# Optimization experiments

Hardware: AMD Instinct MI355X
Metric: run time of the kernel (lower is better)

The kernel has to match this reference:

```python
import jax, jax.numpy as jnp
import numpy as np

N = 10000      # atoms
F = 32         # nr_atom_basis
H = 7          # nr_heads
C = F * H      # nr_coefficients = 224
E = 200000     # edges
NRBF = 50
CUTOFF = 5.0
EPS = 1e-8


def _seg_sum(x, idx, n):
    return jax.ops.segment_sum(x, idx, num_segments=n)


def _seg_mean(x, idx, n):
    # torch scatter_reduce 'mean' with include_self=False: sum/count, 0 for empty segments
    s = _seg_sum(x, idx, n)
    cnt = _seg_sum(jnp.ones((x.shape[0],), x.dtype), idx, n)
    cnt = jnp.maximum(cnt, 1.0).reshape((n,) + (1,) * (x.ndim - 1))
    return s / cnt


def _scatter_softmax(w, idx, n):
    m = jax.ops.segment_max(w, idx, num_segments=n)
    m = jnp.where(jnp.isfinite(m), m, 0.0)  # guard empty segments
    e = jnp.exp(w - m[idx])
    s = _seg_sum(e, idx, n)
    return e / s[idx]


def setup_inputs():
    key = jax.random.key(0)
    ks = jax.random.split(key, 16)
    def w(k, shape, scale=0.1):
        return jax.random.normal(k, shape, jnp.float32) * scale
    return {
        "h": w(ks[0], (N, F), 1.0),
        "x": w(ks[1], (N, 3), 1.0),
        "v": w(ks[2], (N, 3), 0.1),
        "pairlist": jax.random.randint(ks[3], (2, E), 0, N),
        "w_in": w(ks[4], (2 * F, NRBF)), "b_in": jnp.zeros((NRBF,), jnp.float32),
        "w_e1": w(ks[5], (2 * F + NRBF + 1, F)), "b_e1": jnp.zeros((F,), jnp.float32),
        "w_e2": w(ks[6], (F, F)), "b_e2": jnp.zeros((F,), jnp.float32),
        "w_att": w(ks[7], (F, H)), "b_att": jnp.zeros((H,), jnp.float32),
        "w_n1": w(ks[8], (F + C + F, F)), "b_n1": jnp.zeros((F,), jnp.float32),
        "w_n2": w(ks[9], (F, F)), "b_n2": jnp.zeros((F,), jnp.float32),
        "w_pn1": w(ks[10], (C, F)), "b_pn1": jnp.zeros((F,), jnp.float32),
        "w_pn2": w(ks[11], (F, F)), "b_pn2": jnp.zeros((F,), jnp.float32),
        "w_v1": w(ks[12], (F, F)), "b_v1": jnp.zeros((F,), jnp.float32),
        "w_v2": w(ks[13], (F, 1)),
        "w_xmix": w(ks[14], (C, C)),
        "w_vmix": w(ks[15], (C, 1)),
    }


def reference(h, x, v, pairlist, w_in, b_in, w_e1, b_e1, w_e2, b_e2,
              w_att, b_att, w_n1, b_n1, w_n2, b_n2, w_pn1, b_pn1,
              w_pn2, b_pn2, w_v1, b_v1, w_v2, w_xmix, w_vmix):
    act = jax.nn.silu
    idx_i, idx_j = pairlist[0], pairlist[1]
    n = h.shape[0]

    r_ij = x[idx_j] - x[idx_i]                      # [E,3]
    d_ij = jnp.linalg.norm(r_ij, axis=-1)           # [E]
    dir_ij = r_ij / (d_ij[:, None] + EPS)           # [E,3]

    # edge model: continuous-filter conv with concatenation
    h_cat = jnp.concatenate([h[idx_i], h[idx_j]], axis=-1)           # [E,2F]
    centers = jnp.linspace(0.0, CUTOFF, NRBF)
    width = centers[1] - centers[0]
    rbf = jnp.exp(-0.5 * ((d_ij[:, None] - centers) / width) ** 2)   # [E,NRBF]
    filt = rbf * (h_cat @ w_in + b_in)                               # [E,NRBF]
    edge_in = jnp.concatenate([h_cat, filt, d_ij[:, None]], axis=-1)
    h_ij_edge = act(edge_in @ w_e1 + b_e1) @ w_e2 + b_e2             # [E,F]

    # semantic attention (scatter softmax over edges grouped by idx_i)
    att_w = jax.nn.celu(h_ij_edge @ w_att + b_att, alpha=2.0)        # [E,H]
    cut = 0.5 * (jnp.cos(jnp.pi * d_ij / CUTOFF) + 1.0) * (d_ij < CUTOFF)
    att = _scatter_softmax(att_w * cut[:, None], idx_i, n)           # [E,H]
    # einsum('pf,ph->pfh').reshape -> f-major, h-minor
    h_ij_sem = (h_ij_edge[:, :, None] * att[:, None, :]).reshape(-1, C)  # [E,C]
    h_i_sem = _seg_sum(h_ij_sem, idx_i, n)                           # [N,C]

    # equivariant combinations + spatial attention
    comb = jnp.tanh(h_ij_sem @ w_xmix)[:, :, None] * dir_ij[:, None, :]  # [E,C,3]
    comb_mean = _seg_mean(comb, idx_i, n)                            # [N,C,3]
    cnsq = jnp.sum(comb_mean ** 2, axis=-1)                          # [N,C]
    h_i_spatial = act(act(cnsq @ w_pn1 + b_pn1) @ w_pn2 + b_pn2)     # [N,F]

    # node update
    node_in = jnp.concatenate([h, h_i_sem, h_i_spatial], axis=-1)
    h_upd = h + act(act(node_in @ w_n1 + b_n1) @ w_n2 + b_n2)        # [N,F]

    # velocity update
    v_ij = jnp.einsum('ecx,c->ex', comb, w_vmix[:, 0])               # [E,3]
    dv = _seg_mean(v_ij, idx_i, n)                                   # [N,3]
    gate = 2.0 * jax.nn.sigmoid(act(h @ w_v1 + b_v1) @ w_v2)         # [N,1]
    v_upd = gate * v + dv
    x_upd = x + v_upd
    return h_upd, x_upd, v_upd
```

## Files before the change

kernel.cpp:

```cpp
#include <hip/hip_runtime.h>
#include <math.h>

typedef unsigned short u16;
typedef __attribute__((ext_vector_type(8))) short bf16x8;
typedef __attribute__((ext_vector_type(4))) float f32x4;

constexpr int kF    = 32;
constexpr int kH    = 7;
constexpr int kC    = 224;
constexpr int kRBF  = 50;
constexpr int kM    = 128;
constexpr int kStr  = 232;
constexpr int kEM   = 128;
constexpr int kAStr = 136;
constexpr int kBStr = 40;
constexpr float kCut = 5.0f;
constexpr float kEps = 1e-8f;

__device__ __forceinline__ float silu_f(float a) { return a / (1.f + __expf(-a)); }
__device__ __forceinline__ float tanh_f(float x) {
    x = fminf(fmaxf(x, -15.f), 15.f);
    float e = __expf(2.f * x);
    return (e - 1.f) / (e + 1.f);
}
__device__ __forceinline__ float bf2f(u16 u) {
    union { unsigned int i; float f; } v; v.i = ((unsigned int)u) << 16; return v.f;
}
__device__ __forceinline__ u16 f2bf(float f) {
    union { float f; unsigned int i; } v; v.f = f;
    unsigned int x = v.i;
    unsigned int round = ((x >> 16) & 1u) + 0x7fffu;
    return (u16)((x + round) >> 16);
}
__device__ __forceinline__ unsigned pk2(float a, float b) {
    return (unsigned)f2bf(a) | ((unsigned)f2bf(b) << 16);
}

__global__ __launch_bounds__(256) void init_kernel(
    const float* __restrict__ wx, const float* __restrict__ w_in,
    const float* __restrict__ w_e1, const float* __restrict__ w_e2,
    const float* __restrict__ w_att, const float* __restrict__ b_e2,
    const float* __restrict__ b_att,
    u16* __restrict__ wxT, u16* __restrict__ W1T, u16* __restrict__ W2T,
    u16* __restrict__ W3T, u16* __restrict__ W24T, float* __restrict__ b24,
    int* __restrict__ counts, int* __restrict__ cursor, int N_)
{
    int idx = blockIdx.x * 256 + threadIdx.x;
    if (idx < kC * kC) {
        int c = idx / kC, k = idx - c * kC;
        wxT[idx] = f2bf(wx[k * kC + c]);
    }
    if (idx < N_) { counts[idx] = 0; cursor[idx] = 0; }

    if (blockIdx.x == 0) {
        int t = threadIdx.x;
        for (int i = t; i < 64 * 64; i += 256) {
            int n = i >> 6, k = i & 63;
            W1T[i] = f2bf((n < kRBF) ? w_in[k * kRBF + n] : 0.f);
        }
        for (int i = t; i < 32 * 128; i += 256) {
            int n = i >> 7, k = i & 127;
            W2T[i] = f2bf((k < 115) ? w_e1[k * kF + n] : 0.f);
        }
        for (int i = t; i < 32 * 32; i += 256) {
            int n = i >> 5, k = i & 31;
            W3T[i] = f2bf(w_e2[k * kF + n]);
        }
        for (int i = t; i < 16 * 32; i += 256) {
            int n = i >> 5, k = i & 31;
            float a = 0.f;
            if (n < kH) for (int o = 0; o < kF; o++) a += w_e2[k * kF + o] * w_att[o * kH + n];
            W24T[i] = f2bf(a);
        }
        if (t < kH) {
            float a = b_att[t];
            for (int o = 0; o < kF; o++) a += b_e2[o] * w_att[o * kH + t];
            b24[t] = a;
        }
    }
}

__global__ __launch_bounds__(256) void edge_kernel(
    const float* __restrict__ h, const float* __restrict__ x,
    const int* __restrict__ pl, int E_,
    const float* __restrict__ b_in, const float* __restrict__ b_e1,
    const float* __restrict__ b_e2,
    const u16* __restrict__ W1T, const u16* __restrict__ W2T,
    const u16* __restrict__ W3T, const u16* __restrict__ W24T,
    const float* __restrict__ b24,
    float* __restrict__ he_g, float* __restrict__ logit_g,
    float* __restrict__ dir_g, int* __restrict__ counts)
{
    __shared__ __align__(16) u16 s_A[kEM][kAStr];
    __shared__ __align__(16) u16 s_t1[kEM][kBStr];
    __shared__ float s_d[kEM];

    int t = threadIdx.x;
    int T0 = blockIdx.x * kEM;
    int w = t >> 6, lane = t & 63, quad = lane >> 4, l15 = lane & 15;

    {
        int e = t >> 1, half = t & 1;
        int ge = T0 + e;
        bool val = ge < E_;
        int i = 0, j = 0;
        if (val) { i = pl[ge]; j = pl[E_ + ge]; }
        const float4* pi = (const float4*)(h + (size_t)i * kF) + half * 4;
        const float4* pj = (const float4*)(h + (size_t)j * kF) + half * 4;
#pragma unroll
        for (int q = 0; q < 4; q++) {
            float4 a = val ? pi[q] : make_float4(0.f, 0.f, 0.f, 0.f);
            float4 b = val ? pj[q] : make_float4(0.f, 0.f, 0.f, 0.f);
            unsigned* di = (unsigned*)&s_A[e][half * 16 + 4 * q];
            di[0] = pk2(a.x, a.y); di[1] = pk2(a.z, a.w);
            unsigned* dj = (unsigned*)&s_A[e][kF + half * 16 + 4 * q];
            dj[0] = pk2(b.x, b.y); dj[1] = pk2(b.z, b.w);
        }
        if (half == 0) {
            float d = 0.f;
            if (val) {
                float r0 = x[j * 3 + 0] - x[i * 3 + 0];
                float r1 = x[j * 3 + 1] - x[i * 3 + 1];
                float r2 = x[j * 3 + 2] - x[i * 3 + 2];
                d = sqrtf(r0 * r0 + r1 * r1 + r2 * r2);
                float inv = 1.0f / (d + kEps);
                dir_g[(size_t)ge * 3 + 0] = r0 * inv;
                dir_g[(size_t)ge * 3 + 1] = r1 * inv;
                dir_g[(size_t)ge * 3 + 2] = r2 * inv;
                atomicAdd(&counts[i], 1);
            }
            s_d[e] = d;
            s_A[e][114] = f2bf(d);
            s_A[e][115] = 0;
            unsigned* z = (unsigned*)&s_A[e][116];
#pragma unroll
            for (int q = 0; q < 6; q++) z[q] = 0u;
        }
    }
    __syncthreads();

    const float invw = 49.0f / kCut;

    {
        bf16x8 a1[2][2];
#pragma unroll
        for (int rt = 0; rt < 2; rt++)
#pragma unroll
            for (int kt = 0; kt < 2; kt++)
                a1[rt][kt] = *(const bf16x8*)&s_A[32 * w + 16 * rt + l15][kt * 32 + quad * 8];
#pragma unroll
        for (int ct = 0; ct < 4; ct++) {
            int c = ct * 16 + l15;
            bf16x8 b0 = *(const bf16x8*)(W1T + (size_t)c * 64 + quad * 8);
            bf16x8 b1 = *(const bf16x8*)(W1T + (size_t)c * 64 + 32 + quad * 8);
            float bin = (c < kRBF) ? b_in[c] : 0.f;
#pragma unroll
            for (int rt = 0; rt < 2; rt++) {
                f32x4 acc = {0.f, 0.f, 0.f, 0.f};
                acc = __builtin_amdgcn_mfma_f32_16x16x32_bf16(a1[rt][0], b0, acc, 0, 0, 0);
                acc = __builtin_amdgcn_mfma_f32_16x16x32_bf16(a1[rt][1], b1, acc, 0, 0, 0);
                if (c < kRBF) {
#pragma unroll
                    for (int r = 0; r < 4; r++) {
                        int row = 32 * w + 16 * rt + quad * 4 + r;
                        float arg = s_d[row] * invw - (float)c;
                        float filt = __expf(-0.5f * arg * arg) * (acc[r] + bin);
                        s_A[row][64 + c] = f2bf(filt);
                    }
                }
            }
        }
    }

    {
        bf16x8 a2[2][4];
#pragma unroll
        for (int rt = 0; rt < 2; rt++)
#pragma unroll
            for (int kt = 0; kt < 4; kt++)
                a2[rt][kt] = *(const bf16x8*)&s_A[32 * w + 16 * rt + l15][kt * 32 + quad * 8];
#pragma unroll
        for (int ct = 0; ct < 2; ct++) {
            int c = ct * 16 + l15;
            bf16x8 bb[4];
#pragma unroll
            for (int kt = 0; kt < 4; kt++)
                bb[kt] = *(const bf16x8*)(W2T + (size_t)c * 128 + kt * 32 + quad * 8);
            float be = b_e1[c];
#pragma unroll
            for (int rt = 0; rt < 2; rt++) {
                f32x4 acc = {0.f, 0.f, 0.f, 0.f};
#pragma unroll
                for (int kt = 0; kt < 4; kt++)
                    acc = __builtin_amdgcn_mfma_f32_16x16x32_bf16(a2[rt][kt], bb[kt], acc, 0, 0, 0);
#pragma unroll
                for (int r = 0; r < 4; r++) {
                    int row = 32 * w + 16 * rt + quad * 4 + r;
                    s_t1[row][c] = f2bf(silu_f(acc[r] + be));
                }
            }
        }
    }

    {
        bf16x8 a3[2];
#pragma unroll
        for (int rt = 0; rt < 2; rt++)
            a3[rt] = *(const bf16x8*)&s_t1[32 * w + 16 * rt + l15][quad * 8];

#pragma unroll
        for (int ct = 0; ct < 2; ct++) {
            int c = ct * 16 + l15;
            bf16x8 b3 = *(const bf16x8*)(W3T + (size_t)c * 32 + quad * 8);
            float be = b_e2[c];
#pragma unroll
            for (int rt = 0; rt < 2; rt++) {
                f32x4 acc = {0.f, 0.f, 0.f, 0.f};
                acc = __builtin_amdgcn_mfma_f32_16x16x32_bf16(a3[rt], b3, acc, 0, 0, 0);
#pragma unroll
                for (int r = 0; r < 4; r++) {
                    int row = 32 * w + 16 * rt + quad * 4 + r;
                    int ge = T0 + row;
                    if (ge < E_) he_g[(size_t)ge * kF + c] = acc[r] + be;
                }
            }
        }
        {
            bf16x8 b4 = *(const bf16x8*)(W24T + (size_t)l15 * 32 + quad * 8);
            float bb = (l15 < kH) ? b24[l15] : 0.f;
#pragma unroll
            for (int rt = 0; rt < 2; rt++) {
                f32x4 acc = {0.f, 0.f, 0.f, 0.f};
                acc = __builtin_amdgcn_mfma_f32_16x16x32_bf16(a3[rt], b4, acc, 0, 0, 0);
                if (l15 < kH) {
#pragma unroll
                    for (int r = 0; r < 4; r++) {
                        int row = 32 * w + 16 * rt + quad * 4 + r;
                        int ge = T0 + row;
                        if (ge < E_) {
                            float a = acc[r] + bb;
                            a = (a >= 0.f) ? a : 2.f * (__expf(0.5f * a) - 1.f);
                            float dd = s_d[row];
                            float cut = (dd < kCut)
                                ? 0.5f * (__cosf(0.62831853071795864f * dd) + 1.f) : 0.f;
                            logit_g[(size_t)ge * kH + l15] = a * cut;
                        }
                    }
                }
            }
        }
    }
}

__global__ __launch_bounds__(1024) void scan_kernel(
    const int* __restrict__ counts, int* __restrict__ offsets, int n)
{
    __shared__ int buf[1024];
    int t = threadIdx.x;
    int chunk = (n + 1023) >> 10;
    int lo = t * chunk;
    int s = 0;
    for (int i = 0; i < chunk; i++) {
        int g = lo + i;
        if (g < n) s += counts[g];
    }
    buf[t] = s;
    __syncthreads();
    for (int off = 1; off < 1024; off <<= 1) {
        int v = (t >= off) ? buf[t - off] : 0;
        __syncthreads();
        buf[t] += v;
        __syncthreads();
    }
    int run = buf[t] - s;
    for (int i = 0; i < chunk; i++) {
        int g = lo + i;
        if (g < n) { offsets[g] = run; run += counts[g]; }
    }
    if (t == 1023) offsets[n] = buf[1023];
}

__global__ __launch_bounds__(256) void scatter_kernel(
    const int* __restrict__ pl, const int* __restrict__ offsets,
    int* __restrict__ cursor, int* __restrict__ sorted, int E_)
{
    int e = blockIdx.x * 256 + threadIdx.x;
    if (e < E_) {
        int i = pl[e];
        int p = atomicAdd(&cursor[i], 1);
        sorted[offsets[i] + p] = e;
    }
}

__global__ __launch_bounds__(256) void stats_kernel(
    const float* __restrict__ logit_g, const int* __restrict__ offsets,
    const int* __restrict__ sorted,
    float* __restrict__ m_g, float* __restrict__ invs_g, int N_)
{
    int wave = threadIdx.x >> 6;
    int lane = threadIdx.x & 63;
    int node = blockIdx.x * 4 + wave;
    if (node >= N_) return;
    int base = offsets[node];
    int deg  = offsets[node + 1] - base;

    float m[kH], ss[kH];
#pragma unroll
    for (int hh = 0; hh < kH; hh++) { m[hh] = -1e30f; ss[hh] = 0.f; }
    for (int e = lane; e < deg; e += 64) {
        int ed = sorted[base + e];
        const float* lp = logit_g + (size_t)ed * kH;
#pragma unroll
        for (int hh = 0; hh < kH; hh++) {
            float vv = lp[hh];
            if (vv > m[hh]) { ss[hh] *= __expf(m[hh] - vv); m[hh] = vv; }
            ss[hh] += __expf(vv - m[hh]);
        }
    }
#pragma unroll
    for (int hh = 0; hh < kH; hh++) {
        float mm = m[hh], s2 = ss[hh];
#pragma unroll
        for (int off = 32; off >= 1; off >>= 1) {
            float mo = __shfl_xor(mm, off);
            float so = __shfl_xor(s2, off);
            float mn = fmaxf(mm, mo);
            s2 = s2 * __expf(mm - mn) + so * __expf(mo - mn);
            mm = mn;
        }
        if (lane == 0) {
            m_g[(size_t)node * kH + hh] = mm;
            invs_g[(size_t)node * kH + hh] = (s2 > 0.f) ? 1.f / s2 : 0.f;
        }
    }
}

__global__ __launch_bounds__(256) void xmix_kernel(
    const float* __restrict__ he_g, const float* __restrict__ logit_g,
    const float* __restrict__ dir_g,
    const int* __restrict__ pl, const int* __restrict__ sorted,
    const float* __restrict__ m_g, const float* __restrict__ invs_g,
    const u16* __restrict__ wxT, int E_,
    float* __restrict__ nodeacc, float* __restrict__ bpart, int* __restrict__ bid)
{
    __shared__ __align__(16) u16 s_buf[kM][kStr];
    __shared__ float s_att[kM][kH];
    __shared__ __align__(16) float s_dir4[kM][4];
    __shared__ int   s_ed[kM];
    __shared__ int   s_node[kM];
    __shared__ int   s_prev, s_next;

    int t = threadIdx.x;
    int T0 = blockIdx.x * kM;
    int cp = min(kM, E_ - T0);

    if (t < kM) {
        int gi = T0 + t;
        int ed = (gi < E_) ? sorted[gi] : -1;
        s_ed[t] = ed;
        s_node[t] = (ed >= 0) ? pl[ed] : -1;
    }
    if (t == 0) {
        s_prev = (T0 > 0) ? pl[sorted[T0 - 1]] : -2;
        s_next = (T0 + cp < E_) ? pl[sorted[T0 + cp]] : -2;
    }
    __syncthreads();

    int w    = t >> 6;
    int lane = t & 63;
    int quad = lane >> 4;
    int l15  = lane & 15;

    int ws = 32 * w;
    int we = min(ws + 32, cp);
    bool winvalid = (ws < cp);
    bool contL = false, contR = false;
    if (winvalid) {
        int nfirst = s_node[ws], nlast = s_node[we - 1];
        contL = (w == 0) ? (s_prev == nfirst) : (s_node[ws - 1] == nfirst);
        contR = (we == cp) ? (s_next == nlast) : (s_node[we] == nlast);
    }
    if (lane == 0) {
        int b0 = -1, b1 = -1;
        if (winvalid) {
            int nfirst = s_node[ws], nlast = s_node[we - 1];
            b0 = contL ? nfirst : -1;
            if (contR && !(nfirst == nlast && contL)) b1 = nlast;
        }
        bid[8 * blockIdx.x + 2 * w + 0] = b0;
        bid[8 * blockIdx.x + 2 * w + 1] = b1;
    }
    bool active_w = winvalid && (lane < 56);
    int c0 = 4 * lane;

    for (int idx = t; idx < kM * kH; idx += 256) {
        int e = idx / kH, hh = idx - e * kH;
        int ed = s_ed[e];
        float a = 0.f;
        if (ed >= 0) {
            int nd = s_node[e];
            a = __expf(logit_g[(size_t)ed * kH + hh] - m_g[(size_t)nd * kH + hh])
                * invs_g[(size_t)nd * kH + hh];
        }
        s_att[e][hh] = a;
    }
    for (int idx = t; idx < cp * 3; idx += 256) {
        int e = idx / 3, xx = idx - e * 3;
        s_dir4[e][xx] = dir_g[(size_t)s_ed[e] * 3 + xx];
    }
    __syncthreads();

#pragma unroll
    for (int p = 0; p < kM * kF / 256; p++) {
        int idx = t + 256 * p;
        int e = idx >> 5, f = idx & 31;
        int ed = s_ed[e];
        float hv = (ed >= 0) ? he_g[(size_t)ed * kF + f] : 0.f;
        u16 sw[7];
#pragma unroll
        for (int hh = 0; hh < kH; hh++) sw[hh] = f2bf(hv * s_att[e][hh]);
        u16* dst = &s_buf[e][f * 7];
        if ((f & 1) == 0) {
            *(unsigned int*)(dst)     = (unsigned int)sw[0] | ((unsigned int)sw[1] << 16);
            *(unsigned int*)(dst + 2) = (unsigned int)sw[2] | ((unsigned int)sw[3] << 16);
            *(unsigned int*)(dst + 4) = (unsigned int)sw[4] | ((unsigned int)sw[5] << 16);
            dst[6] = sw[6];
        } else {
            dst[0] = sw[0];
            *(unsigned int*)(dst + 1) = (unsigned int)sw[1] | ((unsigned int)sw[2] << 16);
            *(unsigned int*)(dst + 3) = (unsigned int)sw[3] | ((unsigned int)sw[4] << 16);
            *(unsigned int*)(dst + 5) = (unsigned int)sw[5] | ((unsigned int)sw[6] << 16);
        }
    }
    __syncthreads();

    if (active_w) {
        float hs0 = 0.f, hs1 = 0.f, hs2 = 0.f, hs3 = 0.f;
        int rs = ws;
        for (int e = ws; e < we; e++) {
            if (s_node[e] != s_node[rs]) {
                bool comp = (rs > ws) || !contL;
                float4 vv = make_float4(hs0, hs1, hs2, hs3);
                if (comp) *(float4*)&nodeacc[(size_t)s_node[rs] * 896 + 672 + c0] = vv;
                else *(float4*)&bpart[(size_t)(8 * blockIdx.x + 2 * w) * 896 + 672 + c0] = vv;
                hs0 = hs1 = hs2 = hs3 = 0.f; rs = e;
            }
            uint2 pv = *(const uint2*)&s_buf[e][c0];
            hs0 += bf2f((u16)pv.x); hs1 += bf2f((u16)(pv.x >> 16));
            hs2 += bf2f((u16)pv.y); hs3 += bf2f((u16)(pv.y >> 16));
        }
        bool t0 = (rs == ws);
        bool comp = ((!t0) || !contL) && !contR;
        float4 vv = make_float4(hs0, hs1, hs2, hs3);
        if (comp) *(float4*)&nodeacc[(size_t)s_node[rs] * 896 + 672 + c0] = vv;
        else {
            int slot = (t0 && contL) ? 0 : 1;
            *(float4*)&bpart[(size_t)(8 * blockIdx.x + 2 * w + slot) * 896 + 672 + c0] = vv;
        }
    }

    bf16x8 afr[2][7];
#pragma unroll
    for (int rt = 0; rt < 2; rt++)
#pragma unroll
        for (int kt = 0; kt < 7; kt++)
            afr[rt][kt] = *(const bf16x8*)&s_buf[32 * w + 16 * rt + l15][kt * 32 + quad * 8];

    bf16x8 bA[7], bB[7];
    {
        const u16* bp = wxT + (size_t)l15 * kC + quad * 8;
#pragma unroll
        for (int kt = 0; kt < 7; kt++) bA[kt] = *(const bf16x8*)(bp + kt * 32);
    }
    __syncthreads();

    for (int ct = 0; ct < 14; ct++) {
        bf16x8* cur = (ct & 1) ? bB : bA;
        bf16x8* nxt = (ct & 1) ? bA : bB;
        if (ct < 13) {
            const u16* bp = wxT + (size_t)((ct + 1) * 16 + l15) * kC + quad * 8;
#pragma unroll
            for (int kt = 0; kt < 7; kt++) nxt[kt] = *(const bf16x8*)(bp + kt * 32);
        }
        f32x4 acc0 = {0.f, 0.f, 0.f, 0.f};
        f32x4 acc1 = {0.f, 0.f, 0.f, 0.f};
#pragma unroll
        for (int kt = 0; kt < 7; kt++) {
            acc0 = __builtin_amdgcn_mfma_f32_16x16x32_bf16(afr[0][kt], cur[kt], acc0, 0, 0, 0);
            acc1 = __builtin_amdgcn_mfma_f32_16x16x32_bf16(afr[1][kt], cur[kt], acc1, 0, 0, 0);
        }
        int colg = ct * 16 + l15;
#pragma unroll
        for (int s = 0; s < 2; s++) {
            f32x4 ac = s ? acc1 : acc0;
            int rbase = 32 * w + 16 * s + quad * 4;
#pragma unroll
            for (int r = 0; r < 4; r++)
                s_buf[rbase + r][colg] = f2bf(tanh_f(ac[r]));
        }
    }
    __syncthreads();

    if (active_w) {
        float a0[4] = {0.f, 0.f, 0.f, 0.f};
        float a1[4] = {0.f, 0.f, 0.f, 0.f};
        float a2[4] = {0.f, 0.f, 0.f, 0.f};
        int rs = ws;
        for (int e = ws; e < we; e++) {
            if (s_node[e] != s_node[rs]) {
                bool comp = (rs > ws) || !contL;
                float* p = comp ? (nodeacc + (size_t)s_node[rs] * 896)
                                : (bpart + (size_t)(8 * blockIdx.x + 2 * w) * 896);
                *(float4*)&p[c0]       = make_float4(a0[0], a0[1], a0[2], a0[3]);
                *(float4*)&p[224 + c0] = make_float4(a1[0], a1[1], a1[2], a1[3]);
                *(float4*)&p[448 + c0] = make_float4(a2[0], a2[1], a2[2], a2[3]);
#pragma unroll
                for (int q = 0; q < 4; q++) { a0[q] = 0.f; a1[q] = 0.f; a2[q] = 0.f; }
                rs = e;
            }
            float4 dd = *(const float4*)&s_dir4[e][0];
            uint2 pv = *(const uint2*)&s_buf[e][c0];
            float Tv[4];
            Tv[0] = bf2f((u16)pv.x); Tv[1] = bf2f((u16)(pv.x >> 16));
            Tv[2] = bf2f((u16)pv.y); Tv[3] = bf2f((u16)(pv.y >> 16));
#pragma unroll
            for (int q = 0; q < 4; q++) {
                a0[q] += Tv[q] * dd.x;
                a1[q] += Tv[q] * dd.y;
                a2[q] += Tv[q] * dd.z;
            }
        }
        bool t0 = (rs == ws);
        bool comp = ((!t0) || !contL) && !contR;
        float* p;
        if (comp) p = nodeacc + (size_t)s_node[rs] * 896;
        else {
            int slot = (t0 && contL) ? 0 : 1;
            p = bpart + (size_t)(8 * blockIdx.x + 2 * w + slot) * 896;
        }
        *(float4*)&p[c0]       = make_float4(a0[0], a0[1], a0[2], a0[3]);
        *(float4*)&p[224 + c0] = make_float4(a1[0], a1[1], a1[2], a1[3]);
        *(float4*)&p[448 + c0] = make_float4(a2[0], a2[1], a2[2], a2[3]);
    }
}

__global__ __launch_bounds__(256) void node_kernel(
    const float* __restrict__ h, const float* __restrict__ x, const float* __restrict__ v,
    const float* __restrict__ nodeacc, const float* __restrict__ bpart,
    const int* __restrict__ bid, const int* __restrict__ offs,
    const float* __restrict__ w_n1, const float* __restrict__ b_n1,
    const float* __restrict__ w_n2, const float* __restrict__ b_n2,
    const float* __restrict__ w_pn1, const float* __restrict__ b_pn1,
    const float* __restrict__ w_pn2, const float* __restrict__ b_pn2,
    const float* __restrict__ w_v1, const float* __restrict__ b_v1,
    const float* __restrict__ w_v2, const float* __restrict__ w_vmix,
    float* __restrict__ out_h, float* __restrict__ out_x, float* __restrict__ out_v,
    int N_)
{
    __shared__ float s_cm[4][3][kC];
    __shared__ float s_cnsq[4][kC];
    __shared__ float s_ni[4][288];
    __shared__ float s_part[8][4][kF];
    __shared__ float s_hn[4][kF], s_sp1[4][kF], s_spat[4][kF], s_n1v[4][kF], s_g1[4][kF];
    __shared__ float s_pdv[4][3][8];
    __shared__ float s_gate[4], s_dv[4][3];

    int t = threadIdx.x;
    int n0 = blockIdx.x * 4;

    if (t < kC) {
        for (int nd = 0; nd < 4; nd++) {
            int node = n0 + nd;
            if (node >= N_) break;
            int base = offs[node], end = offs[node + 1];
            int deg = end - base;
            float a0 = 0.f, a1 = 0.f, a2 = 0.f, hh = 0.f;
            if (deg > 0) {
                int wlo = base >> 5, whi = (end - 1) >> 5;
                if (wlo == whi) {
                    const float* p = nodeacc + (size_t)node * 896;
                    a0 = p[t]; a1 = p[224 + t]; a2 = p[448 + t]; hh = p[672 + t];
                } else {
                    for (int W = wlo; W <= whi; W++) {
#pragma unroll
                        for (int s = 0; s < 2; s++) {
                            if (bid[2 * W + s] == node) {
                                const float* p = bpart + (size_t)(2 * W + s) * 896;
                                a0 += p[t]; a1 += p[224 + t]; a2 += p[448 + t]; hh += p[672 + t];
                            }
                        }
                    }
                }
            }
            float invc = 1.f / fmaxf((float)deg, 1.f);
            float m0 = a0 * invc, m1 = a1 * invc, m2 = a2 * invc;
            s_cm[nd][0][t] = m0; s_cm[nd][1][t] = m1; s_cm[nd][2][t] = m2;
            s_cnsq[nd][t] = m0 * m0 + m1 * m1 + m2 * m2;
            s_ni[nd][kF + t] = hh;
        }
    } else {
        int ln = t - 224;
        for (int nd = 0; nd < 4; nd++) {
            int node = n0 + nd;
            float hv = (node < N_) ? h[(size_t)node * kF + ln] : 0.f;
            s_hn[nd][ln] = hv;
            s_ni[nd][ln] = hv;
        }
    }
    __syncthreads();

    int o = t & 31, g = t >> 5;
    {
        float acc[4] = {0.f, 0.f, 0.f, 0.f};
        int cb = g * 28;
        for (int i = 0; i < 28; i++) {
            float wv = w_pn1[(cb + i) * kF + o];
#pragma unroll
            for (int nd = 0; nd < 4; nd++) acc[nd] += s_cnsq[nd][cb + i] * wv;
        }
#pragma unroll
        for (int nd = 0; nd < 4; nd++) s_part[g][nd][o] = acc[nd];
    }
    __syncthreads();
    if (t < 128) {
        int nd = t >> 5;
        float a = b_pn1[o];
#pragma unroll
        for (int g2 = 0; g2 < 8; g2++) a += s_part[g2][nd][o];
        s_sp1[nd][o] = silu_f(a);
    } else {
        int nd = (t - 128) >> 5;
        float a = b_v1[o];
        for (int f = 0; f < kF; f++) a += s_hn[nd][f] * w_v1[f * kF + o];
        s_g1[nd][o] = silu_f(a);
    }
    __syncthreads();
    if (t < 128) {
        int nd = t >> 5;
        float a = b_pn2[o];
        for (int o2 = 0; o2 < kF; o2++) a += s_sp1[nd][o2] * w_pn2[o2 * kF + o];
        s_spat[nd][o] = silu_f(a);
    } else if (t < 132) {
        int nd = t - 128;
        float a = 0.f;
        for (int o2 = 0; o2 < kF; o2++) a += s_g1[nd][o2] * w_v2[o2];
        s_gate[nd] = 2.f / (1.f + __expf(-a));
    } else if (t >= 160) {
        int q = t - 160; int nd = q / 24; int r = q - nd * 24;
        int xx = r >> 3, ln = r & 7;
        float a = 0.f;
        for (int c = ln; c < kC; c += 8) a += w_vmix[c] * s_cm[nd][xx][c];
        s_pdv[nd][xx][ln] = a;
    }
    __syncthreads();
    if (t < 128) {
        int nd = t >> 5;
        s_ni[nd][kF + kC + o] = s_spat[nd][o];
    } else if (t < 140) {
        int q = t - 128; int nd = q / 3; int xx = q - nd * 3;
        float a = 0.f;
#pragma unroll
        for (int ln = 0; ln < 8; ln++) a += s_pdv[nd][xx][ln];
        s_dv[nd][xx] = a;
    }
    __syncthreads();
    {
        float acc[4] = {0.f, 0.f, 0.f, 0.f};
        int rb = g * 36;
        for (int i = 0; i < 36; i++) {
            float wv = w_n1[(rb + i) * kF + o];
#pragma unroll
            for (int nd = 0; nd < 4; nd++) acc[nd] += s_ni[nd][rb + i] * wv;
        }
#pragma unroll
        for (int nd = 0; nd < 4; nd++) s_part[g][nd][o] = acc[nd];
    }
    __syncthreads();
    if (t < 128) {
        int nd = t >> 5;
        float a = b_n1[o];
#pragma unroll
        for (int g2 = 0; g2 < 8; g2++) a += s_part[g2][nd][o];
        s_n1v[nd][o] = silu_f(a);
    }
    __syncthreads();
    if (t < 128) {
        int nd = t >> 5; int node = n0 + nd;
        if (node < N_) {
            float a = b_n2[o];
            for (int o2 = 0; o2 < kF; o2++) a += s_n1v[nd][o2] * w_n2[o2 * kF + o];
            out_h[(size_t)node * kF + o] = s_hn[nd][o] + silu_f(a);
        }
    } else if (t < 140) {
        int q = t - 128; int nd = q / 3; int xx = q - nd * 3;
        int node = n0 + nd;
        if (node < N_) {
            float vv = v[(size_t)node * 3 + xx];
            float vu = s_gate[nd] * vv + s_dv[nd][xx];
            out_v[(size_t)node * 3 + xx] = vu;
            out_x[(size_t)node * 3 + xx] = x[(size_t)node * 3 + xx] + vu;
        }
    }
}

extern "C" void kernel_launch(void* const* d_in, const int* in_sizes, int n_in,
                              void* d_out, int out_size, void* d_ws, size_t ws_size,
                              hipStream_t stream)
{
    const float* h      = (const float*)d_in[0];
    const float* x      = (const float*)d_in[1];
    const float* v      = (const float*)d_in[2];
    const int*   pl     = (const int*)d_in[3];
    const float* w_in   = (const float*)d_in[4];
    const float* b_in   = (const float*)d_in[5];
    const float* w_e1   = (const float*)d_in[6];
    const float* b_e1   = (const float*)d_in[7];
    const float* w_e2   = (const float*)d_in[8];
    const float* b_e2   = (const float*)d_in[9];
    const float* w_att  = (const float*)d_in[10];
    const float* b_att  = (const float*)d_in[11];
    const float* w_n1   = (const float*)d_in[12];
    const float* b_n1   = (const float*)d_in[13];
    const float* w_n2   = (const float*)d_in[14];
    const float* b_n2   = (const float*)d_in[15];
    const float* w_pn1  = (const float*)d_in[16];
    const float* b_pn1  = (const float*)d_in[17];
    const float* w_pn2  = (const float*)d_in[18];
    const float* b_pn2  = (const float*)d_in[19];
    const float* w_v1   = (const float*)d_in[20];
    const float* b_v1   = (const float*)d_in[21];
    const float* w_v2   = (const float*)d_in[22];
    const float* w_xmix = (const float*)d_in[23];
    const float* w_vmix = (const float*)d_in[24];

    const int E_ = in_sizes[3] / 2;
    const int N_ = in_sizes[0] / kF;
    const int nblk = (E_ + kM - 1) / kM;

    char* w = (char*)d_ws;
    u16*   wxT     = (u16*)w;   w += (size_t)kC * kC * 2;
    u16*   W1T     = (u16*)w;   w += (size_t)64 * 64 * 2;
    u16*   W2T     = (u16*)w;   w += (size_t)32 * 128 * 2;
    u16*   W3T     = (u16*)w;   w += (size_t)32 * 32 * 2;
    u16*   W24T    = (u16*)w;   w += (size_t)16 * 32 * 2;
    float* b24     = (float*)w; w += 8 * 4;
    float* he_g    = (float*)w; w += (size_t)E_ * kF * 4;
    float* logit_g = (float*)w; w += (size_t)E_ * kH * 4;
    float* dir_g   = (float*)w; w += (size_t)E_ * 3 * 4;
    float* m_g     = (float*)w; w += (size_t)N_ * kH * 4;
    float* invs_g  = (float*)w; w += (size_t)N_ * kH * 4;
    float* nodeacc = (float*)w; w += (size_t)N_ * 896 * 4;
    float* bpart   = (float*)w; w += (size_t)8 * nblk * 896 * 4;
    int*   bid     = (int*)w;   w += (size_t)8 * nblk * 4;
    int* counts    = (int*)w;   w += (size_t)N_ * 4;
    int* offs      = (int*)w;   w += (size_t)(N_ + 1) * 4;
    int* cursor    = (int*)w;   w += (size_t)N_ * 4;
    int* sorted    = (int*)w;   w += (size_t)E_ * 4;

    float* out_h = (float*)d_out;
    float* out_x = out_h + (size_t)N_ * kF;
    float* out_v = out_x + (size_t)N_ * 3;

    init_kernel<<<dim3((kC * kC + 255) / 256), dim3(256), 0, stream>>>(
        w_xmix, w_in, w_e1, w_e2, w_att, b_e2, b_att,
        wxT, W1T, W2T, W3T, W24T, b24, counts, cursor, N_);

    edge_kernel<<<dim3((E_ + kEM - 1) / kEM), dim3(256), 0, stream>>>(
        h, x, pl, E_, b_in, b_e1, b_e2, W1T, W2T, W3T, W24T, b24,
        he_g, logit_g, dir_g, counts);

    scan_kernel<<<dim3(1), dim3(1024), 0, stream>>>(counts, offs, N_);

    scatter_kernel<<<dim3((E_ + 255) / 256), dim3(256), 0, stream>>>(
        pl, offs, cursor, sorted, E_);

    stats_kernel<<<dim3((N_ + 3) / 4), dim3(256), 0, stream>>>(
        logit_g, offs, sorted, m_g, invs_g, N_);

    xmix_kernel<<<dim3(nblk), dim3(256), 0, stream>>>(
        he_g, logit_g, dir_g, pl, sorted, m_g, invs_g, wxT, E_,
        nodeacc, bpart, bid);

    node_kernel<<<dim3((N_ + 3) / 4), dim3(256), 0, stream>>>(
        h, x, v, nodeacc, bpart, bid, offs,
        w_n1, b_n1, w_n2, b_n2, w_pn1, b_pn1, w_pn2, b_pn2,
        w_v1, b_v1, w_v2, w_vmix, out_h, out_x, out_v, N_);
}
```

Baseline: 361.7 us.

## Halve xmix tile to 64 edges per block and raise occupancy

Shrinks the xmix_kernel edge tile from 128 to 64 rows and drops the padded LDS stride. Each wave's MFMA A-fragment falls from two row tiles to one, and only two waves own segment windows. A launch bound of 5 blocks per SM is added to get more resident blocks, and bpart/bid are resized for two windows per block. tanh is simplified to drop the clamp, and bf16 packing uses the HIP intrinsic, trading some B-fragment reuse and adding LDS bank conflicts for lower per-block footprint.

```diff
diff --git a/kernel.cpp b/kernel.cpp
--- a/kernel.cpp
+++ b/kernel.cpp
@@ -1,4 +1,5 @@
 #include <hip/hip_runtime.h>
+#include <hip/hip_bf16.h>
 #include <math.h>
 
 typedef unsigned short u16;
@@ -9,8 +10,8 @@
 constexpr int kH    = 7;
 constexpr int kC    = 224;
 constexpr int kRBF  = 50;
-constexpr int kM    = 128;
-constexpr int kStr  = 232;
+constexpr int kM    = 64;
+constexpr int kStr  = 224;
 constexpr int kEM   = 128;
 constexpr int kAStr = 136;
 constexpr int kBStr = 40;
@@ -19,9 +20,8 @@
 
 __device__ __forceinline__ float silu_f(float a) { return a / (1.f + __expf(-a)); }
 __device__ __forceinline__ float tanh_f(float x) {
-    x = fminf(fmaxf(x, -15.f), 15.f);
     float e = __expf(2.f * x);
-    return (e - 1.f) / (e + 1.f);
+    return 1.f - 2.f / (e + 1.f);
 }
 __device__ __forceinline__ float bf2f(u16 u) {
     union { unsigned int i; float f; } v; v.i = ((unsigned int)u) << 16; return v.f;
@@ -33,7 +33,9 @@
     return (u16)((x + round) >> 16);
 }
 __device__ __forceinline__ unsigned pk2(float a, float b) {
-    return (unsigned)f2bf(a) | ((unsigned)f2bf(b) << 16);
+    union { __hip_bfloat162 h; unsigned u; } v;
+    v.h = __float22bfloat162_rn(make_float2(a, b));
+    return v.u;
 }
 
 __global__ __launch_bounds__(256) void init_kernel(
@@ -335,7 +337,7 @@
     }
 }
 
-__global__ __launch_bounds__(256) void xmix_kernel(
+__global__ __launch_bounds__(256, 5) void xmix_kernel(
     const float* __restrict__ he_g, const float* __restrict__ logit_g,
     const float* __restrict__ dir_g,
     const int* __restrict__ pl, const int* __restrict__ sorted,
@@ -373,22 +375,23 @@
 
     int ws = 32 * w;
     int we = min(ws + 32, cp);
-    bool winvalid = (ws < cp);
+    bool winvalid = (w < 2) && (ws < cp);
     bool contL = false, contR = false;
     if (winvalid) {
         int nfirst = s_node[ws], nlast = s_node[we - 1];
         contL = (w == 0) ? (s_prev == nfirst) : (s_node[ws - 1] == nfirst);
         contR = (we == cp) ? (s_next == nlast) : (s_node[we] == nlast);
     }
-    if (lane == 0) {
+    if (w < 2 && lane == 0) {
         int b0 = -1, b1 = -1;
         if (winvalid) {
             int nfirst = s_node[ws], nlast = s_node[we - 1];
             b0 = contL ? nfirst : -1;
             if (contR && !(nfirst == nlast && contL)) b1 = nlast;
         }
-        bid[8 * blockIdx.x + 2 * w + 0] = b0;
-        bid[8 * blockIdx.x + 2 * w + 1] = b1;
+        int gw = 2 * blockIdx.x + w;
+        bid[2 * gw + 0] = b0;
+        bid[2 * gw + 1] = b1;
     }
     bool active_w = winvalid && (lane < 56);
     int c0 = 4 * lane;
@@ -416,20 +419,20 @@
         int e = idx >> 5, f = idx & 31;
         int ed = s_ed[e];
         float hv = (ed >= 0) ? he_g[(size_t)ed * kF + f] : 0.f;
-        u16 sw[7];
-#pragma unroll
-        for (int hh = 0; hh < kH; hh++) sw[hh] = f2bf(hv * s_att[e][hh]);
+        float sv[7];
+#pragma unroll
+        for (int hh = 0; hh < kH; hh++) sv[hh] = hv * s_att[e][hh];
         u16* dst = &s_buf[e][f * 7];
         if ((f & 1) == 0) {
-            *(unsigned int*)(dst)     = (unsigned int)sw[0] | ((unsigned int)sw[1] << 16);
-            *(unsigned int*)(dst + 2) = (unsigned int)sw[2] | ((unsigned int)sw[3] << 16);
-            *(unsigned int*)(dst + 4) = (unsigned int)sw[4] | ((unsigned int)sw[5] << 16);
-            dst[6] = sw[6];
+            *(unsigned*)(dst)     = pk2(sv[0], sv[1]);
+            *(unsigned*)(dst + 2) = pk2(sv[2], sv[3]);
+            *(unsigned*)(dst + 4) = pk2(sv[4], sv[5]);
+            dst[6] = f2bf(sv[6]);
         } else {
-            dst[0] = sw[0];
-            *(unsigned int*)(dst + 1) = (unsigned int)sw[1] | ((unsigned int)sw[2] << 16);
-            *(unsigned int*)(dst + 3) = (unsigned int)sw[3] | ((unsigned int)sw[4] << 16);
-            *(unsigned int*)(dst + 5) = (unsigned int)sw[5] | ((unsigned int)sw[6] << 16);
+            dst[0] = f2bf(sv[0]);
+            *(unsigned*)(dst + 1) = pk2(sv[1], sv[2]);
+            *(unsigned*)(dst + 3) = pk2(sv[3], sv[4]);
+            *(unsigned*)(dst + 5) = pk2(sv[5], sv[6]);
         }
     }
     __syncthreads();
@@ -441,8 +444,9 @@
             if (s_node[e] != s_node[rs]) {
                 bool comp = (rs > ws) || !contL;
                 float4 vv = make_float4(hs0, hs1, hs2, hs3);
+                int gw = 2 * blockIdx.x + w;
                 if (comp) *(float4*)&nodeacc[(size_t)s_node[rs] * 896 + 672 + c0] = vv;
-                else *(float4*)&bpart[(size_t)(8 * blockIdx.x + 2 * w) * 896 + 672 + c0] = vv;
+                else *(float4*)&bpart[(size_t)(2 * gw) * 896 + 672 + c0] = vv;
                 hs0 = hs1 = hs2 = hs3 = 0.f; rs = e;
             }
             uint2 pv = *(const uint2*)&s_buf[e][c0];
@@ -455,16 +459,15 @@
         if (comp) *(float4*)&nodeacc[(size_t)s_node[rs] * 896 + 672 + c0] = vv;
         else {
             int slot = (t0 && contL) ? 0 : 1;
-            *(float4*)&bpart[(size_t)(8 * blockIdx.x + 2 * w + slot) * 896 + 672 + c0] = vv;
-        }
-    }
-
-    bf16x8 afr[2][7];
-#pragma unroll
-    for (int rt = 0; rt < 2; rt++)
-#pragma unroll
-        for (int kt = 0; kt < 7; kt++)
-            afr[rt][kt] = *(const bf16x8*)&s_buf[32 * w + 16 * rt + l15][kt * 32 + quad * 8];
+            int gw = 2 * blockIdx.x + w;
+            *(float4*)&bpart[(size_t)(2 * gw + slot) * 896 + 672 + c0] = vv;
+        }
+    }
+
+    bf16x8 afr[7];
+#pragma unroll
+    for (int kt = 0; kt < 7; kt++)
+        afr[kt] = *(const bf16x8*)&s_buf[16 * w + l15][kt * 32 + quad * 8];
 
     bf16x8 bA[7], bB[7];
     {
@@ -482,22 +485,18 @@
 #pragma unroll
             for (int kt = 0; kt < 7; kt++) nxt[kt] = *(const bf16x8*)(bp + kt * 32);
         }
-        f32x4 acc0 = {0.f, 0.f, 0.f, 0.f};
-        f32x4 acc1 = {0.f, 0.f, 0.f, 0.f};
-#pragma unroll
-        for (int kt = 0; kt < 7; kt++) {
-            acc0 = __builtin_amdgcn_mfma_f32_16x16x32_bf16(afr[0][kt], cur[kt], acc0, 0, 0, 0);
-            acc1 = __builtin_amdgcn_mfma_f32_16x16x32_bf16(afr[1][kt], cur[kt], acc1, 0, 0, 0);
-        }
+        f32x4 acc = {0.f, 0.f, 0.f, 0.f};
+#pragma unroll
+        for (int kt = 0; kt < 7; kt++)
+            acc = __builtin_amdgcn_mfma_f32_16x16x32_bf16(afr[kt], cur[kt], acc, 0, 0, 0);
         int colg = ct * 16 + l15;
-#pragma unroll
-        for (int s = 0; s < 2; s++) {
-            f32x4 ac = s ? acc1 : acc0;
-            int rbase = 32 * w + 16 * s + quad * 4;
-#pragma unroll
-            for (int r = 0; r < 4; r++)
-                s_buf[rbase + r][colg] = f2bf(tanh_f(ac[r]));
-        }
+        int rbase = 16 * w + quad * 4;
+        unsigned p01 = pk2(tanh_f(acc[0]), tanh_f(acc[1]));
+        unsigned p23 = pk2(tanh_f(acc[2]), tanh_f(acc[3]));
+        s_buf[rbase + 0][colg] = (u16)p01;
+        s_buf[rbase + 1][colg] = (u16)(p01 >> 16);
+        s_buf[rbase + 2][colg] = (u16)p23;
+        s_buf[rbase + 3][colg] = (u16)(p23 >> 16);
     }
     __syncthreads();
 
@@ -506,11 +505,12 @@
         float a1[4] = {0.f, 0.f, 0.f, 0.f};
         float a2[4] = {0.f, 0.f, 0.f, 0.f};
         int rs = ws;
+        int gw = 2 * blockIdx.x + w;
         for (int e = ws; e < we; e++) {
             if (s_node[e] != s_node[rs]) {
                 bool comp = (rs > ws) || !contL;
                 float* p = comp ? (nodeacc + (size_t)s_node[rs] * 896)
-                                : (bpart + (size_t)(8 * blockIdx.x + 2 * w) * 896);
+                                : (bpart + (size_t)(2 * gw) * 896);
                 *(float4*)&p[c0]       = make_float4(a0[0], a0[1], a0[2], a0[3]);
                 *(float4*)&p[224 + c0] = make_float4(a1[0], a1[1], a1[2], a1[3]);
                 *(float4*)&p[448 + c0] = make_float4(a2[0], a2[1], a2[2], a2[3]);
@@ -536,7 +536,7 @@
         if (comp) p = nodeacc + (size_t)s_node[rs] * 896;
         else {
             int slot = (t0 && contL) ? 0 : 1;
-            p = bpart + (size_t)(8 * blockIdx.x + 2 * w + slot) * 896;
+            p = bpart + (size_t)(2 * gw + slot) * 896;
         }
         *(float4*)&p[c0]       = make_float4(a0[0], a0[1], a0[2], a0[3]);
         *(float4*)&p[224 + c0] = make_float4(a1[0], a1[1], a1[2], a1[3]);
@@ -750,8 +750,8 @@
     float* m_g     = (float*)w; w += (size_t)N_ * kH * 4;
     float* invs_g  = (float*)w; w += (size_t)N_ * kH * 4;
     float* nodeacc = (float*)w; w += (size_t)N_ * 896 * 4;
-    float* bpart   = (float*)w; w += (size_t)8 * nblk * 896 * 4;
-    int*   bid     = (int*)w;   w += (size_t)8 * nblk * 4;
+    float* bpart   = (float*)w; w += (size_t)4 * nblk * 896 * 4;
+    int*   bid     = (int*)w;   w += (size_t)4 * nblk * 4;
     int* counts    = (int*)w;   w += (size_t)N_ * 4;
     int* offs      = (int*)w;   w += (size_t)(N_ + 1) * 4;
     int* cursor    = (int*)w;   w += (size_t)N_ * 4;
```

After: 381.5 us. 1.05x slower.

## Sort edges before edge MLP and write edge outputs in sorted order

Applied to the files above, without the earlier changes.

A separate histogram kernel now builds per-node counts, and the scan and scatter run before the edge kernel. The scatter produces a per-edge rank and a sorted node-id array. The edge kernel writes he, logit and dir directly at the sorted position, so stats and xmix read contiguously instead of gathering through an indirection array. This adds one extra pass over the pairlist and turns the edge kernel stores into scattered writes. It also simplifies tanh (the clamp is dropped) and uses packed bf16 conversion intrinsics.

```diff
diff --git a/kernel.cpp b/kernel.cpp
--- a/kernel.cpp
+++ b/kernel.cpp
@@ -1,4 +1,5 @@
 #include <hip/hip_runtime.h>
+#include <hip/hip_bf16.h>
 #include <math.h>
 
 typedef unsigned short u16;
@@ -19,9 +20,8 @@
 
 __device__ __forceinline__ float silu_f(float a) { return a / (1.f + __expf(-a)); }
 __device__ __forceinline__ float tanh_f(float x) {
-    x = fminf(fmaxf(x, -15.f), 15.f);
     float e = __expf(2.f * x);
-    return (e - 1.f) / (e + 1.f);
+    return 1.f - 2.f / (e + 1.f);
 }
 __device__ __forceinline__ float bf2f(u16 u) {
     union { unsigned int i; float f; } v; v.i = ((unsigned int)u) << 16; return v.f;
@@ -33,7 +33,9 @@
     return (u16)((x + round) >> 16);
 }
 __device__ __forceinline__ unsigned pk2(float a, float b) {
-    return (unsigned)f2bf(a) | ((unsigned)f2bf(b) << 16);
+    union { __hip_bfloat162 h; unsigned u; } v;
+    v.h = __float22bfloat162_rn(make_float2(a, b));
+    return v.u;
 }
 
 __global__ __launch_bounds__(256) void init_kernel(
@@ -80,20 +82,70 @@
     }
 }
 
+__global__ __launch_bounds__(256) void hist_kernel(
+    const int* __restrict__ pl, int* __restrict__ counts, int E_)
+{
+    int e = blockIdx.x * 256 + threadIdx.x;
+    if (e < E_) atomicAdd(&counts[pl[e]], 1);
+}
+
+__global__ __launch_bounds__(1024) void scan_kernel(
+    const int* __restrict__ counts, int* __restrict__ offsets, int n)
+{
+    __shared__ int buf[1024];
+    int t = threadIdx.x;
+    int chunk = (n + 1023) >> 10;
+    int lo = t * chunk;
+    int s = 0;
+    for (int i = 0; i < chunk; i++) {
+        int g = lo + i;
+        if (g < n) s += counts[g];
+    }
+    buf[t] = s;
+    __syncthreads();
+    for (int off = 1; off < 1024; off <<= 1) {
+        int v = (t >= off) ? buf[t - off] : 0;
+        __syncthreads();
+        buf[t] += v;
+        __syncthreads();
+    }
+    int run = buf[t] - s;
+    for (int i = 0; i < chunk; i++) {
+        int g = lo + i;
+        if (g < n) { offsets[g] = run; run += counts[g]; }
+    }
+    if (t == 1023) offsets[n] = buf[1023];
+}
+
+__global__ __launch_bounds__(256) void scatter_kernel(
+    const int* __restrict__ pl, const int* __restrict__ offsets,
+    int* __restrict__ cursor, int* __restrict__ rank, int* __restrict__ nid, int E_)
+{
+    int e = blockIdx.x * 256 + threadIdx.x;
+    if (e < E_) {
+        int i = pl[e];
+        int p = atomicAdd(&cursor[i], 1);
+        int pos = offsets[i] + p;
+        rank[e] = pos;
+        nid[pos] = i;
+    }
+}
+
 __global__ __launch_bounds__(256) void edge_kernel(
     const float* __restrict__ h, const float* __restrict__ x,
-    const int* __restrict__ pl, int E_,
+    const int* __restrict__ pl, const int* __restrict__ rank_g, int E_,
     const float* __restrict__ b_in, const float* __restrict__ b_e1,
     const float* __restrict__ b_e2,
     const u16* __restrict__ W1T, const u16* __restrict__ W2T,
     const u16* __restrict__ W3T, const u16* __restrict__ W24T,
     const float* __restrict__ b24,
     float* __restrict__ he_g, float* __restrict__ logit_g,
-    float* __restrict__ dir_g, int* __restrict__ counts)
+    float* __restrict__ dir_g)
 {
     __shared__ __align__(16) u16 s_A[kEM][kAStr];
     __shared__ __align__(16) u16 s_t1[kEM][kBStr];
     __shared__ float s_d[kEM];
+    __shared__ int   s_r[kEM];
 
     int t = threadIdx.x;
     int T0 = blockIdx.x * kEM;
@@ -118,17 +170,19 @@
         }
         if (half == 0) {
             float d = 0.f;
+            int r = 0;
             if (val) {
+                r = rank_g[ge];
                 float r0 = x[j * 3 + 0] - x[i * 3 + 0];
                 float r1 = x[j * 3 + 1] - x[i * 3 + 1];
                 float r2 = x[j * 3 + 2] - x[i * 3 + 2];
                 d = sqrtf(r0 * r0 + r1 * r1 + r2 * r2);
                 float inv = 1.0f / (d + kEps);
-                dir_g[(size_t)ge * 3 + 0] = r0 * inv;
-                dir_g[(size_t)ge * 3 + 1] = r1 * inv;
-                dir_g[(size_t)ge * 3 + 2] = r2 * inv;
-                atomicAdd(&counts[i], 1);
-            }
+                dir_g[(size_t)r * 3 + 0] = r0 * inv;
+                dir_g[(size_t)r * 3 + 1] = r1 * inv;
+                dir_g[(size_t)r * 3 + 2] = r2 * inv;
+            }
+            s_r[e] = r;
             s_d[e] = d;
             s_A[e][114] = f2bf(d);
             s_A[e][115] = 0;
@@ -221,7 +275,7 @@
                 for (int r = 0; r < 4; r++) {
                     int row = 32 * w + 16 * rt + quad * 4 + r;
                     int ge = T0 + row;
-                    if (ge < E_) he_g[(size_t)ge * kF + c] = acc[r] + be;
+                    if (ge < E_) he_g[(size_t)s_r[row] * kF + c] = acc[r] + be;
                 }
             }
         }
@@ -243,7 +297,7 @@
                             float dd = s_d[row];
                             float cut = (dd < kCut)
                                 ? 0.5f * (__cosf(0.62831853071795864f * dd) + 1.f) : 0.f;
-                            logit_g[(size_t)ge * kH + l15] = a * cut;
+                            logit_g[(size_t)s_r[row] * kH + l15] = a * cut;
                         }
                     }
                 }
@@ -252,49 +306,8 @@
     }
 }
 
-__global__ __launch_bounds__(1024) void scan_kernel(
-    const int* __restrict__ counts, int* __restrict__ offsets, int n)
-{
-    __shared__ int buf[1024];
-    int t = threadIdx.x;
-    int chunk = (n + 1023) >> 10;
-    int lo = t * chunk;
-    int s = 0;
-    for (int i = 0; i < chunk; i++) {
-        int g = lo + i;
-        if (g < n) s += counts[g];
-    }
-    buf[t] = s;
-    __syncthreads();
-    for (int off = 1; off < 1024; off <<= 1) {
-        int v = (t >= off) ? buf[t - off] : 0;
-        __syncthreads();
-        buf[t] += v;
-        __syncthreads();
-    }
-    int run = buf[t] - s;
-    for (int i = 0; i < chunk; i++) {
-        int g = lo + i;
-        if (g < n) { offsets[g] = run; run += counts[g]; }
-    }
-    if (t == 1023) offsets[n] = buf[1023];
-}
-
-__global__ __launch_bounds__(256) void scatter_kernel(
-    const int* __restrict__ pl, const int* __restrict__ offsets,
-    int* __restrict__ cursor, int* __restrict__ sorted, int E_)
-{
-    int e = blockIdx.x * 256 + threadIdx.x;
-    if (e < E_) {
-        int i = pl[e];
-        int p = atomicAdd(&cursor[i], 1);
-        sorted[offsets[i] + p] = e;
-    }
-}
-
 __global__ __launch_bounds__(256) void stats_kernel(
     const float* __restrict__ logit_g, const int* __restrict__ offsets,
-    const int* __restrict__ sorted,
     float* __restrict__ m_g, float* __restrict__ invs_g, int N_)
 {
     int wave = threadIdx.x >> 6;
@@ -308,8 +321,7 @@
 #pragma unroll
     for (int hh = 0; hh < kH; hh++) { m[hh] = -1e30f; ss[hh] = 0.f; }
     for (int e = lane; e < deg; e += 64) {
-        int ed = sorted[base + e];
-        const float* lp = logit_g + (size_t)ed * kH;
+        const float* lp = logit_g + (size_t)(base + e) * kH;
 #pragma unroll
         for (int hh = 0; hh < kH; hh++) {
             float vv = lp[hh];
@@ -337,8 +349,7 @@
 
 __global__ __launch_bounds__(256) void xmix_kernel(
     const float* __restrict__ he_g, const float* __restrict__ logit_g,
-    const float* __restrict__ dir_g,
-    const int* __restrict__ pl, const int* __restrict__ sorted,
+    const float* __restrict__ dir_g, const int* __restrict__ nid,
     const float* __restrict__ m_g, const float* __restrict__ invs_g,
     const u16* __restrict__ wxT, int E_,
     float* __restrict__ nodeacc, float* __restrict__ bpart, int* __restrict__ bid)
@@ -346,7 +357,6 @@
     __shared__ __align__(16) u16 s_buf[kM][kStr];
     __shared__ float s_att[kM][kH];
     __shared__ __align__(16) float s_dir4[kM][4];
-    __shared__ int   s_ed[kM];
     __shared__ int   s_node[kM];
     __shared__ int   s_prev, s_next;
 
@@ -354,15 +364,10 @@
     int T0 = blockIdx.x * kM;
     int cp = min(kM, E_ - T0);
 
-    if (t < kM) {
-        int gi = T0 + t;
-        int ed = (gi < E_) ? sorted[gi] : -1;
-        s_ed[t] = ed;
-        s_node[t] = (ed >= 0) ? pl[ed] : -1;
-    }
+    if (t < kM) s_node[t] = (T0 + t < E_) ? nid[T0 + t] : -1;
     if (t == 0) {
-        s_prev = (T0 > 0) ? pl[sorted[T0 - 1]] : -2;
-        s_next = (T0 + cp < E_) ? pl[sorted[T0 + cp]] : -2;
+        s_prev = (T0 > 0) ? nid[T0 - 1] : -2;
+        s_next = (T0 + cp < E_) ? nid[T0 + cp] : -2;
     }
     __syncthreads();
 
@@ -395,18 +400,17 @@
 
     for (int idx = t; idx < kM * kH; idx += 256) {
         int e = idx / kH, hh = idx - e * kH;
-        int ed = s_ed[e];
         float a = 0.f;
-        if (ed >= 0) {
+        if (T0 + e < E_) {
             int nd = s_node[e];
-            a = __expf(logit_g[(size_t)ed * kH + hh] - m_g[(size_t)nd * kH + hh])
+            a = __expf(logit_g[(size_t)(T0 + e) * kH + hh] - m_g[(size_t)nd * kH + hh])
                 * invs_g[(size_t)nd * kH + hh];
         }
         s_att[e][hh] = a;
     }
     for (int idx = t; idx < cp * 3; idx += 256) {
         int e = idx / 3, xx = idx - e * 3;
-        s_dir4[e][xx] = dir_g[(size_t)s_ed[e] * 3 + xx];
+        s_dir4[e][xx] = dir_g[(size_t)(T0 + e) * 3 + xx];
     }
     __syncthreads();
 
@@ -414,22 +418,21 @@
     for (int p = 0; p < kM * kF / 256; p++) {
         int idx = t + 256 * p;
         int e = idx >> 5, f = idx & 31;
-        int ed = s_ed[e];
-        float hv = (ed >= 0) ? he_g[(size_t)ed * kF + f] : 0.f;
-        u16 sw[7];
-#pragma unroll
-        for (int hh = 0; hh < kH; hh++) sw[hh] = f2bf(hv * s_att[e][hh]);
+        float hv = (T0 + e < E_) ? he_g[(size_t)(T0 + e) * kF + f] : 0.f;
+        float sv[7];
+#pragma unroll
+        for (int hh = 0; hh < kH; hh++) sv[hh] = hv * s_att[e][hh];
         u16* dst = &s_buf[e][f * 7];
         if ((f & 1) == 0) {
-            *(unsigned int*)(dst)     = (unsigned int)sw[0] | ((unsigned int)sw[1] << 16);
-            *(unsigned int*)(dst + 2) = (unsigned int)sw[2] | ((unsigned int)sw[3] << 16);
-            *(unsigned int*)(dst + 4) = (unsigned int)sw[4] | ((unsigned int)sw[5] << 16);
-            dst[6] = sw[6];
+            *(unsigned*)(dst)     = pk2(sv[0], sv[1]);
+            *(unsigned*)(dst + 2) = pk2(sv[2], sv[3]);
+            *(unsigned*)(dst + 4) = pk2(sv[4], sv[5]);
+            dst[6] = f2bf(sv[6]);
         } else {
-            dst[0] = sw[0];
-            *(unsigned int*)(dst + 1) = (unsigned int)sw[1] | ((unsigned int)sw[2] << 16);
-            *(unsigned int*)(dst + 3) = (unsigned int)sw[3] | ((unsigned int)sw[4] << 16);
-            *(unsigned int*)(dst + 5) = (unsigned int)sw[5] | ((unsigned int)sw[6] << 16);
+            dst[0] = f2bf(sv[0]);
+            *(unsigned*)(dst + 1) = pk2(sv[1], sv[2]);
+            *(unsigned*)(dst + 3) = pk2(sv[3], sv[4]);
+            *(unsigned*)(dst + 5) = pk2(sv[5], sv[6]);
         }
     }
     __syncthreads();
@@ -494,9 +497,12 @@
         for (int s = 0; s < 2; s++) {
             f32x4 ac = s ? acc1 : acc0;
             int rbase = 32 * w + 16 * s + quad * 4;
-#pragma unroll
-            for (int r = 0; r < 4; r++)
-                s_buf[rbase + r][colg] = f2bf(tanh_f(ac[r]));
+            unsigned p01 = pk2(tanh_f(ac[0]), tanh_f(ac[1]));
+            unsigned p23 = pk2(tanh_f(ac[2]), tanh_f(ac[3]));
+            s_buf[rbase + 0][colg] = (u16)p01;
+            s_buf[rbase + 1][colg] = (u16)(p01 >> 16);
+            s_buf[rbase + 2][colg] = (u16)p23;
+            s_buf[rbase + 3][colg] = (u16)(p23 >> 16);
         }
     }
     __syncthreads();
@@ -755,7 +761,8 @@
     int* counts    = (int*)w;   w += (size_t)N_ * 4;
     int* offs      = (int*)w;   w += (size_t)(N_ + 1) * 4;
     int* cursor    = (int*)w;   w += (size_t)N_ * 4;
-    int* sorted    = (int*)w;   w += (size_t)E_ * 4;
+    int* rank_g    = (int*)w;   w += (size_t)E_ * 4;
+    int* nid       = (int*)w;   w += (size_t)E_ * 4;
 
     float* out_h = (float*)d_out;
     float* out_x = out_h + (size_t)N_ * kF;
@@ -765,20 +772,22 @@
         w_xmix, w_in, w_e1, w_e2, w_att, b_e2, b_att,
         wxT, W1T, W2T, W3T, W24T, b24, counts, cursor, N_);
 
+    hist_kernel<<<dim3((E_ + 255) / 256), dim3(256), 0, stream>>>(pl, counts, E_);
+
+    scan_kernel<<<dim3(1), dim3(1024), 0, stream>>>(counts, offs, N_);
+
+    scatter_kernel<<<dim3((E_ + 255) / 256), dim3(256), 0, stream>>>(
+        pl, offs, cursor, rank_g, nid, E_);
+
     edge_kernel<<<dim3((E_ + kEM - 1) / kEM), dim3(256), 0, stream>>>(
-        h, x, pl, E_, b_in, b_e1, b_e2, W1T, W2T, W3T, W24T, b24,
-        he_g, logit_g, dir_g, counts);
-
-    scan_kernel<<<dim3(1), dim3(1024), 0, stream>>>(counts, offs, N_);
-
-    scatter_kernel<<<dim3((E_ + 255) / 256), dim3(256), 0, stream>>>(
-        pl, offs, cursor, sorted, E_);
+        h, x, pl, rank_g, E_, b_in, b_e1, b_e2, W1T, W2T, W3T, W24T, b24,
+        he_g, logit_g, dir_g);
 
     stats_kernel<<<dim3((N_ + 3) / 4), dim3(256), 0, stream>>>(
-        logit_g, offs, sorted, m_g, invs_g, N_);
+        logit_g, offs, m_g, invs_g, N_);
 
     xmix_kernel<<<dim3(nblk), dim3(256), 0, stream>>>(
-        he_g, logit_g, dir_g, pl, sorted, m_g, invs_g, wxT, E_,
+        he_g, logit_g, dir_g, nid, m_g, invs_g, wxT, E_,
         nodeacc, bpart, bid);
 
     node_kernel<<<dim3((N_ + 3) / 4), dim3(256), 0, stream>>>(
```

Result: no change. 361.6 us (-0.0%).
